# Optimization experiments

Measured on AMD Instinct MI355X. Metric: run time of the kernel, lower is better.

The kernel has to match this reference:

```python
import jax, jax.numpy as jnp
import numpy as np

B, C, H, W = 4, 512, 64, 64
C8 = C // 8


def setup_inputs() -> dict:
    key = jax.random.key(0)
    ks = jax.random.split(key, 12)
    s = lambda fan_in: 1.0 / np.sqrt(fan_in)
    return {
        "final_encoded": jax.random.normal(ks[0], (B, C, H, W), jnp.float32),
        "total": jax.random.normal(ks[1], (B, C, H, W), jnp.float32),
        # 1x1 conv weights (out, in) and biases
        "Wq": jax.random.normal(ks[2], (C8, C), jnp.float32) * s(C),
        "bq": jax.random.normal(ks[3], (C8,), jnp.float32) * s(C),
        "Wk": jax.random.normal(ks[4], (C8, C), jnp.float32) * s(C),
        "bk": jax.random.normal(ks[5], (C8,), jnp.float32) * s(C),
        "Wv": jax.random.normal(ks[6], (C, C), jnp.float32) * s(C),
        "bv": jax.random.normal(ks[7], (C,), jnp.float32) * s(C),
        # learned additive positional tensors
        "height_tensor": jax.random.normal(ks[8], (1, C8, H, 1), jnp.float32),
        "width_tensor": jax.random.normal(ks[9], (1, C8, 1, W), jnp.float32),
        "gamma": jnp.zeros((1,), jnp.float32),
    }


def reference(final_encoded, total, Wq, bq, Wk, bk, Wv, bv, height_tensor, width_tensor, gamma):
    b, c, h, w = final_encoded.shape
    c8 = c // 8
    hw = h * w
    # 1x1 convs as channel matmuls
    q = jnp.einsum("oc,bchw->bohw", Wq, total) + bq[None, :, None, None]
    k = jnp.einsum("oc,bchw->bohw", Wk, final_encoded) + bk[None, :, None, None]
    v = jnp.einsum("oc,bchw->bohw", Wv, final_encoded) + bv[None, :, None, None]
    pq = q.reshape(b, c8, hw).transpose(0, 2, 1)   # [B, HW, C8]
    pk = k.reshape(b, c8, hw)                      # [B, C8, HW]
    pv = v.reshape(b, c, hw)                       # [B, C, HW]
    energy = jnp.einsum("bnc,bcm->bnm", pq, pk)    # [B, HW, HW] content energy
    pos = (height_tensor + width_tensor).reshape(c8, hw)  # [C8, HW] additive positional bias basis
    energy = energy + jnp.einsum("bnc,cm->bnm", pq, pos)
    attention = jax.nn.softmax(energy, axis=-1)
    # out = bmm(value, attention^T)
    out = jnp.einsum("bcm,bnm->bcn", pv, attention).reshape(b, c, h, w)
    return gamma * out + final_encoded
```

## Files before the change

kernel.cpp:

```cpp
#include <hip/hip_runtime.h>
#include <hip/hip_bf16.h>
#include <type_traits>

#define B_   4
#define C_   512
#define C8_  64
#define HW_  4096

typedef short bf16x8 __attribute__((ext_vector_type(8)));
typedef float f32x4  __attribute__((ext_vector_type(4)));

__device__ __forceinline__ unsigned short f2bf(float f) {
  union { unsigned int i; float f; } x; x.f = f;
  unsigned int r = x.i + 0x7fffu + ((x.i >> 16) & 1u);
  return (unsigned short)(r >> 16);
}

#define MFMA(a, b, c) __builtin_amdgcn_mfma_f32_16x16x32_bf16((a), (b), (c), 0, 0, 0)


__global__ __launch_bounds__(256) void proj_kernel(
    const float* __restrict__ total, const float* __restrict__ fe,
    const float* __restrict__ Wq, const float* __restrict__ bq,
    const float* __restrict__ Wk, const float* __restrict__ bk,
    const float* __restrict__ Wv, const float* __restrict__ bv,
    const float* __restrict__ ht, const float* __restrict__ wt,
    unsigned short* __restrict__ Qh, unsigned short* __restrict__ Kh,
    unsigned short* __restrict__ Vn) {
  __shared__ __align__(16) unsigned short Xs[64 * 72];
  __shared__ __align__(16) unsigned short Ws[128 * 72];
  const int t = threadIdx.x;
  const int b = blockIdx.z;
  const int y = blockIdx.y;
  const int x = blockIdx.x;
  const int m0 = x * 64;
  const int lane = t & 63, w = t >> 6, ln = lane & 15, quad = lane >> 4;

  if (y < 2) {
    const float* X = (y == 0) ? total : fe;
    const float* W = (y == 0) ? Wq : Wk;
    const float* bias = (y == 0) ? bq : bk;
    unsigned short* dst = (y == 0) ? Qh : Kh;

    f32x4 acc[4];
#pragma unroll
    for (int i = 0; i < 4; ++i) acc[i] = f32x4{0.f, 0.f, 0.f, 0.f};

    for (int kb = 0; kb < 8; ++kb) {
      const int c0 = kb * 64;
#pragma unroll
      for (int i = 0; i < 4; ++i) {
        int idx = t + i * 256; int o = idx >> 4, c4 = idx & 15;
        float4 wv = *(const float4*)&W[(size_t)o * C_ + c0 + c4 * 4];
        unsigned int p0 = f2bf(wv.x) | ((unsigned int)f2bf(wv.y) << 16);
        unsigned int p1 = f2bf(wv.z) | ((unsigned int)f2bf(wv.w) << 16);
        *(uint2*)&Ws[o * 72 + c4 * 4] = make_uint2(p0, p1);
      }
#pragma unroll
      for (int i = 0; i < 4; ++i) {
        int idx = t + i * 256; int rc = idx >> 4, mq = idx & 15;
        float4 xv = *(const float4*)&X[((size_t)b * C_ + c0 + rc) * HW_ + m0 + mq * 4];
        Xs[(mq * 4 + 0) * 72 + rc] = f2bf(xv.x);
        Xs[(mq * 4 + 1) * 72 + rc] = f2bf(xv.y);
        Xs[(mq * 4 + 2) * 72 + rc] = f2bf(xv.z);
        Xs[(mq * 4 + 3) * 72 + rc] = f2bf(xv.w);
      }
      __syncthreads();
      bf16x8 a0 = *(const bf16x8*)&Xs[(w * 16 + ln) * 72 + quad * 8];
      bf16x8 a1 = *(const bf16x8*)&Xs[(w * 16 + ln) * 72 + 32 + quad * 8];
#pragma unroll
      for (int nt = 0; nt < 4; ++nt) {
        bf16x8 b0 = *(const bf16x8*)&Ws[(nt * 16 + ln) * 72 + quad * 8];
        bf16x8 b1 = *(const bf16x8*)&Ws[(nt * 16 + ln) * 72 + 32 + quad * 8];
        acc[nt] = MFMA(a0, b0, acc[nt]);
        acc[nt] = MFMA(a1, b1, acc[nt]);
      }
      __syncthreads();
    }

    const int h = x;
#pragma unroll
    for (int nt = 0; nt < 4; ++nt) {
      const int o = nt * 16 + ln;
      const float bz = bias[o];
      const float hv = (y == 1) ? ht[o * 64 + h] : 0.0f;
#pragma unroll
      for (int r = 0; r < 4; ++r) {
        const int mloc = w * 16 + quad * 4 + r;
        float val = acc[nt][r] + bz + hv;
        if (y == 1) val += wt[o * 64 + mloc];
        const size_t idx = ((size_t)b * 512 + (size_t)(x * 4 + w) * 2 + (nt >> 1)) * 512
                         + ((nt & 1) * 2 + (ln >> 3)) * 128 + (quad * 4 + r) * 8 + (ln & 7);
        dst[idx] = f2bf(val);
      }
    }
  } else {
    const int o0 = (y - 2) * 128;
    f32x4 acc[2][4];
#pragma unroll
    for (int p = 0; p < 2; ++p)
#pragma unroll
      for (int i = 0; i < 4; ++i) acc[p][i] = f32x4{0.f, 0.f, 0.f, 0.f};

    for (int kb = 0; kb < 8; ++kb) {
      const int c0 = kb * 64;
#pragma unroll
      for (int i = 0; i < 8; ++i) {
        int idx = t + i * 256; int o = idx >> 4, c4 = idx & 15;
        float4 wv = *(const float4*)&Wv[(size_t)(o0 + o) * C_ + c0 + c4 * 4];
        unsigned int p0 = f2bf(wv.x) | ((unsigned int)f2bf(wv.y) << 16);
        unsigned int p1 = f2bf(wv.z) | ((unsigned int)f2bf(wv.w) << 16);
        *(uint2*)&Ws[o * 72 + c4 * 4] = make_uint2(p0, p1);
      }
#pragma unroll
      for (int i = 0; i < 4; ++i) {
        int idx = t + i * 256; int rc = idx >> 4, mq = idx & 15;
        float4 xv = *(const float4*)&fe[((size_t)b * C_ + c0 + rc) * HW_ + m0 + mq * 4];
        Xs[(mq * 4 + 0) * 72 + rc] = f2bf(xv.x);
        Xs[(mq * 4 + 1) * 72 + rc] = f2bf(xv.y);
        Xs[(mq * 4 + 2) * 72 + rc] = f2bf(xv.z);
        Xs[(mq * 4 + 3) * 72 + rc] = f2bf(xv.w);
      }
      __syncthreads();
      bf16x8 aW[2][2];
#pragma unroll
      for (int p = 0; p < 2; ++p) {
        aW[p][0] = *(const bf16x8*)&Ws[((w + 4 * p) * 16 + ln) * 72 + quad * 8];
        aW[p][1] = *(const bf16x8*)&Ws[((w + 4 * p) * 16 + ln) * 72 + 32 + quad * 8];
      }
#pragma unroll
      for (int nt = 0; nt < 4; ++nt) {
        bf16x8 b0 = *(const bf16x8*)&Xs[(nt * 16 + ln) * 72 + quad * 8];
        bf16x8 b1 = *(const bf16x8*)&Xs[(nt * 16 + ln) * 72 + 32 + quad * 8];
#pragma unroll
        for (int p = 0; p < 2; ++p) {
          acc[p][nt] = MFMA(aW[p][0], b0, acc[p][nt]);
          acc[p][nt] = MFMA(aW[p][1], b1, acc[p][nt]);
        }
      }
      __syncthreads();
    }

#pragma unroll
    for (int p = 0; p < 2; ++p) {
#pragma unroll
      for (int r = 0; r < 4; ++r) {
        const int cht = (o0 >> 4) + w + 4 * p;
        const float bz = bv[cht * 16 + quad * 4 + r];
#pragma unroll
        for (int nt = 0; nt < 4; ++nt) {
          const size_t idx = (((size_t)b * 32 + cht) * 128 + (size_t)x * 2 + (nt >> 1)) * 512
                           + ((nt & 1) * 2 + (ln >> 3)) * 128 + (quad * 4 + r) * 8 + (ln & 7);
          Vn[idx] = f2bf(acc[p][nt][r] + bz);
        }
      }
    }
  }
}

__global__ __launch_bounds__(512, 4) void flash_kernel(
    const unsigned short* __restrict__ Qh, const unsigned short* __restrict__ Kh,
    const unsigned short* __restrict__ Vn, const float* __restrict__ fe,
    const float* __restrict__ gamma, float* __restrict__ out) {
  __shared__ __align__(16) unsigned short Ps[2][64 * 72];
  __shared__ float Red[2][64];

  const int t = threadIdx.x;
  const int n = blockIdx.x;
  const int xcd = n & 7;
  const int b = xcd & 3;
  const int ch0 = (xcd >> 2) * 256;
  const int q0 = (n >> 3) * 64;
  const int lane = t & 63, w = t >> 6, ln = lane & 15, quad = lane >> 4;
  const int qt = w & 3;
  const int kh = w >> 2;

  const unsigned short* Qb = Qh + (size_t)b * 512 * 512;
  const unsigned short* Kb = Kh + (size_t)b * 512 * 512;
  const unsigned short* Vbase = Vn + ((size_t)b * 32 + (ch0 >> 4)) * (128 * 512);

  const bf16x8 aq0 = *(const bf16x8*)&Qb[((size_t)((q0 >> 4) + qt) * 2 + 0) * 512 + lane * 8];
  const bf16x8 aq1 = *(const bf16x8*)&Qb[((size_t)((q0 >> 4) + qt) * 2 + 1) * 512 + lane * 8];

  float Sacc[4] = {0.f, 0.f, 0.f, 0.f};
  f32x4 acc[2][4];
#pragma unroll
  for (int mt = 0; mt < 2; ++mt)
#pragma unroll
    for (int nt = 0; nt < 4; ++nt) acc[mt][nt] = f32x4{0.f, 0.f, 0.f, 0.f};

  bf16x8 kf[2][2];
  bf16x8 vf[2][2];

  auto loadK = [&](int it) {
#pragma unroll
    for (int nt = 0; nt < 2; ++nt)
#pragma unroll
      for (int hf = 0; hf < 2; ++hf)
        kf[nt][hf] = *(const bf16x8*)&Kb[((size_t)(it * 4 + kh * 2 + nt) * 2 + hf) * 512 + lane * 8];
  };
  auto loadV = [&](int it) {
#pragma unroll
    for (int mt = 0; mt < 2; ++mt)
#pragma unroll
      for (int kc = 0; kc < 2; ++kc)
        vf[mt][kc] = *(const bf16x8*)&Vbase[(((size_t)(w * 2 + mt)) * 128 + it * 2 + kc) * 512 + lane * 8];
  };

  loadK(0);
  loadV(0);

  for (int it = 0; it < 64; ++it) {
    unsigned short* Pcur = Ps[it & 1];
    __builtin_amdgcn_s_setprio(1);
    f32x4 e0 = MFMA(aq0, kf[0][0], (f32x4{0.f, 0.f, 0.f, 0.f}));
    e0 = MFMA(aq1, kf[0][1], e0);
    f32x4 e1 = MFMA(aq0, kf[1][0], (f32x4{0.f, 0.f, 0.f, 0.f}));
    e1 = MFMA(aq1, kf[1][1], e1);
    __builtin_amdgcn_s_setprio(0);
    if (it < 63) loadK(it + 1);
#pragma unroll
    for (int r = 0; r < 4; ++r) {
      const float p0 = __expf(e0[r] - 20.0f);
      const float p1 = __expf(e1[r] - 20.0f);
      Sacc[r] += p0 + p1;
      const int qrow = qt * 16 + quad * 4 + r;
      Pcur[qrow * 72 + kh * 32 + ln] = f2bf(p0);
      Pcur[qrow * 72 + kh * 32 + 16 + ln] = f2bf(p1);
    }
    asm volatile("s_waitcnt lgkmcnt(0)" ::: "memory");
    __builtin_amdgcn_s_barrier();
    asm volatile("" ::: "memory");
#pragma unroll
    for (int kc = 0; kc < 2; ++kc) {
      bf16x8 bp[4];
#pragma unroll
      for (int nt = 0; nt < 4; ++nt)
        bp[nt] = *(const bf16x8*)&Pcur[(nt * 16 + ln) * 72 + kc * 32 + quad * 8];
      __builtin_amdgcn_s_setprio(1);
#pragma unroll
      for (int mt = 0; mt < 2; ++mt)
#pragma unroll
        for (int nt = 0; nt < 4; ++nt)
          acc[mt][nt] = MFMA(vf[mt][kc], bp[nt], acc[mt][nt]);
      __builtin_amdgcn_s_setprio(0);
    }
    if (it < 63) loadV(it + 1);
  }

#pragma unroll
  for (int r = 0; r < 4; ++r) {
    float s = Sacc[r];
    s += __shfl_xor(s, 1, 16);
    s += __shfl_xor(s, 2, 16);
    s += __shfl_xor(s, 4, 16);
    s += __shfl_xor(s, 8, 16);
    if (ln == 0) Red[kh][qt * 16 + quad * 4 + r] = s;
  }
  __syncthreads();
  float rsv[4];
#pragma unroll
  for (int nt = 0; nt < 4; ++nt)
    rsv[nt] = 1.0f / (Red[0][nt * 16 + ln] + Red[1][nt * 16 + ln]);

  const float g = gamma[0];
#pragma unroll
  for (int mt = 0; mt < 2; ++mt) {
#pragma unroll
    for (int r = 0; r < 4; ++r) {
      const int ch = ch0 + w * 32 + mt * 16 + quad * 4 + r;
      const size_t base = ((size_t)b * C_ + ch) * HW_ + q0;
#pragma unroll
      for (int nt = 0; nt < 4; ++nt) {
        const size_t idx = base + nt * 16 + ln;
        out[idx] = g * (acc[mt][nt][r] * rsv[nt]) + fe[idx];
      }
    }
  }
}

extern "C" void kernel_launch(void* const* d_in, const int* in_sizes, int n_in,
                              void* d_out, int out_size, void* d_ws, size_t ws_size,
                              hipStream_t stream) {
  const float* fe    = (const float*)d_in[0];
  const float* total = (const float*)d_in[1];
  const float* Wq    = (const float*)d_in[2];
  const float* bq    = (const float*)d_in[3];
  const float* Wk    = (const float*)d_in[4];
  const float* bk    = (const float*)d_in[5];
  const float* Wv    = (const float*)d_in[6];
  const float* bv    = (const float*)d_in[7];
  const float* ht    = (const float*)d_in[8];
  const float* wt    = (const float*)d_in[9];
  const float* gamma = (const float*)d_in[10];
  float* out = (float*)d_out;

  unsigned short* Qh = (unsigned short*)d_ws;
  unsigned short* Kh = Qh + (size_t)B_ * HW_ * C8_;
  unsigned short* Vn = Kh + (size_t)B_ * HW_ * C8_;

  proj_kernel<<<dim3(64, 6, B_), 256, 0, stream>>>(total, fe, Wq, bq, Wk, bk,
                                                   Wv, bv, ht, wt, Qh, Kh, Vn);
  flash_kernel<<<dim3(512), 512, 0, stream>>>(Qh, Kh, Vn, fe, gamma, out);
}
```

Before: 271.3 us.

## Transpose QK MFMA output and write packed swizzled P tiles to LDS

Swaps the MFMA operand order so each lane holds four consecutive key columns for one query row. This lets the P tile be written as packed bf16 pairs (v_cvt_pk_bf16_f32) in 8-byte stores instead of scalar 2-byte stores. The padded LDS layout is replaced by an XOR-swizzled unpadded one to avoid bank conflicts. The row-sum reduction shrinks to two cross-quad shuffles. It cuts LDS store instruction count and conversion cost, but depends on the swizzle being consistent between writes and reads.

Result: faster. 262.9 us (-3.1%).

```diff
diff --git a/kernel.cpp b/kernel.cpp
--- a/kernel.cpp
+++ b/kernel.cpp
@@ -14,6 +14,12 @@
   union { unsigned int i; float f; } x; x.f = f;
   unsigned int r = x.i + 0x7fffu + ((x.i >> 16) & 1u);
   return (unsigned short)(r >> 16);
+}
+
+__device__ __forceinline__ unsigned int cvtpk(float lo, float hi) {
+  unsigned int r;
+  asm("v_cvt_pk_bf16_f32 %0, %1, %2" : "=v"(r) : "v"(lo), "v"(hi));
+  return r;
 }
 
 #define MFMA(a, b, c) __builtin_amdgcn_mfma_f32_16x16x32_bf16((a), (b), (c), 0, 0, 0)
@@ -162,7 +168,7 @@
     const unsigned short* __restrict__ Qh, const unsigned short* __restrict__ Kh,
     const unsigned short* __restrict__ Vn, const float* __restrict__ fe,
     const float* __restrict__ gamma, float* __restrict__ out) {
-  __shared__ __align__(16) unsigned short Ps[2][64 * 72];
+  __shared__ __align__(16) unsigned short Ps[2][64 * 64];
   __shared__ float Red[2][64];
 
   const int t = threadIdx.x;
@@ -174,6 +180,7 @@
   const int lane = t & 63, w = t >> 6, ln = lane & 15, quad = lane >> 4;
   const int qt = w & 3;
   const int kh = w >> 2;
+  const int swz = (ln & 7) << 4;
 
   const unsigned short* Qb = Qh + (size_t)b * 512 * 512;
   const unsigned short* Kb = Kh + (size_t)b * 512 * 512;
@@ -182,7 +189,7 @@
   const bf16x8 aq0 = *(const bf16x8*)&Qb[((size_t)((q0 >> 4) + qt) * 2 + 0) * 512 + lane * 8];
   const bf16x8 aq1 = *(const bf16x8*)&Qb[((size_t)((q0 >> 4) + qt) * 2 + 1) * 512 + lane * 8];
 
-  float Sacc[4] = {0.f, 0.f, 0.f, 0.f};
+  float Sacc = 0.f;
   f32x4 acc[2][4];
 #pragma unroll
   for (int mt = 0; mt < 2; ++mt)
@@ -210,23 +217,28 @@
   loadK(0);
   loadV(0);
 
+  const int qrow = qt * 16 + ln;
+
   for (int it = 0; it < 64; ++it) {
-    unsigned short* Pcur = Ps[it & 1];
+    char* Pcur = (char*)Ps[it & 1];
     __builtin_amdgcn_s_setprio(1);
-    f32x4 e0 = MFMA(aq0, kf[0][0], (f32x4{0.f, 0.f, 0.f, 0.f}));
-    e0 = MFMA(aq1, kf[0][1], e0);
-    f32x4 e1 = MFMA(aq0, kf[1][0], (f32x4{0.f, 0.f, 0.f, 0.f}));
-    e1 = MFMA(aq1, kf[1][1], e1);
+    f32x4 e0 = MFMA(kf[0][0], aq0, (f32x4{0.f, 0.f, 0.f, 0.f}));
+    e0 = MFMA(kf[0][1], aq1, e0);
+    f32x4 e1 = MFMA(kf[1][0], aq0, (f32x4{0.f, 0.f, 0.f, 0.f}));
+    e1 = MFMA(kf[1][1], aq1, e1);
     __builtin_amdgcn_s_setprio(0);
     if (it < 63) loadK(it + 1);
-#pragma unroll
-    for (int r = 0; r < 4; ++r) {
-      const float p0 = __expf(e0[r] - 20.0f);
-      const float p1 = __expf(e1[r] - 20.0f);
-      Sacc[r] += p0 + p1;
-      const int qrow = qt * 16 + quad * 4 + r;
-      Pcur[qrow * 72 + kh * 32 + ln] = f2bf(p0);
-      Pcur[qrow * 72 + kh * 32 + 16 + ln] = f2bf(p1);
+    {
+      const float p0 = __expf(e0[0] - 20.0f), p1 = __expf(e0[1] - 20.0f);
+      const float p2 = __expf(e0[2] - 20.0f), p3 = __expf(e0[3] - 20.0f);
+      Sacc += (p0 + p1) + (p2 + p3);
+      *(uint2*)(Pcur + ((qrow * 128 + kh * 64 + 0 * 32 + quad * 8) ^ swz)) =
+          make_uint2(cvtpk(p0, p1), cvtpk(p2, p3));
+      const float s0 = __expf(e1[0] - 20.0f), s1 = __expf(e1[1] - 20.0f);
+      const float s2 = __expf(e1[2] - 20.0f), s3 = __expf(e1[3] - 20.0f);
+      Sacc += (s0 + s1) + (s2 + s3);
+      *(uint2*)(Pcur + ((qrow * 128 + kh * 64 + 1 * 32 + quad * 8) ^ swz)) =
+          make_uint2(cvtpk(s0, s1), cvtpk(s2, s3));
     }
     asm volatile("s_waitcnt lgkmcnt(0)" ::: "memory");
     __builtin_amdgcn_s_barrier();
@@ -236,7 +248,7 @@
       bf16x8 bp[4];
 #pragma unroll
       for (int nt = 0; nt < 4; ++nt)
-        bp[nt] = *(const bf16x8*)&Pcur[(nt * 16 + ln) * 72 + kc * 32 + quad * 8];
+        bp[nt] = *(const bf16x8*)(Pcur + ((((nt * 16 + ln) * 128 + kc * 64 + quad * 16)) ^ swz));
       __builtin_amdgcn_s_setprio(1);
 #pragma unroll
       for (int mt = 0; mt < 2; ++mt)
@@ -248,14 +260,11 @@
     if (it < 63) loadV(it + 1);
   }
 
-#pragma unroll
-  for (int r = 0; r < 4; ++r) {
-    float s = Sacc[r];
-    s += __shfl_xor(s, 1, 16);
-    s += __shfl_xor(s, 2, 16);
-    s += __shfl_xor(s, 4, 16);
-    s += __shfl_xor(s, 8, 16);
-    if (ln == 0) Red[kh][qt * 16 + quad * 4 + r] = s;
+  {
+    float s = Sacc;
+    s += __shfl_xor(s, 16);
+    s += __shfl_xor(s, 32);
+    if (quad == 0) Red[kh][qrow] = s;
   }
   __syncthreads();
   float rsv[4];
```
